# Kernel optimization log

Measured on AMD Instinct MI355X. Metric: run time of the kernel, lower is better.

The kernel has to match this reference:

```python
import jax, jax.numpy as jnp
import numpy as np

H, D = 12, 128          # heads, head_dim
DIM = 1536              # vid_dim == txt_dim == H*D
EPS = 1e-6


def _rmsnorm(x, w):
    # RMSNorm over last dim (head_dim) with learnable scale
    var = jnp.mean(jnp.square(x), axis=-1, keepdims=True)
    return x * jax.lax.rsqrt(var + EPS) * w


def setup_inputs() -> dict:
    key = jax.random.key(0)
    ks = jax.random.split(key, 16)
    B, Lv, Lt = 2, 2 * 24 * 40, 128
    inner = H * D
    s = 0.02
    inp = {
        "vid": jax.random.normal(ks[0], (B * Lv, DIM), jnp.float32),
        "txt": jax.random.normal(ks[1], (B * Lt, DIM), jnp.float32),
        "Wqkv_vid": jax.random.normal(ks[2], (DIM, 3 * inner), jnp.float32) * s,
        "bqkv_vid": jnp.zeros((3 * inner,), jnp.float32),
        "Wqkv_txt": jax.random.normal(ks[3], (DIM, 3 * inner), jnp.float32) * s,
        "bqkv_txt": jnp.zeros((3 * inner,), jnp.float32),
        "nq_vid": jnp.ones((D,), jnp.float32),
        "nk_vid": jnp.ones((D,), jnp.float32),
        "nq_txt": jnp.ones((D,), jnp.float32),
        "nk_txt": jnp.ones((D,), jnp.float32),
        "Wout_vid": jax.random.normal(ks[4], (inner, DIM), jnp.float32) * s,
        "bout_vid": jnp.zeros((DIM,), jnp.float32),
        "Wout_txt": jax.random.normal(ks[5], (inner, DIM), jnp.float32) * s,
        "bout_txt": jnp.zeros((DIM,), jnp.float32),
        # static per-sample shapes (numpy => usable as Python ints under jit)
        "vid_shape": np.array([[2, 24, 40], [2, 24, 40]], np.int64),
        "txt_shape": np.array([[128], [128]], np.int64),
    }
    return inp


def reference(vid, txt, Wqkv_vid, bqkv_vid, Wqkv_txt, bqkv_txt,
              nq_vid, nk_vid, nq_txt, nk_txt,
              Wout_vid, bout_vid, Wout_txt, bout_txt,
              vid_shape, txt_shape):
    B = vid_shape.shape[0]
    Lv = int(np.prod(vid_shape[0]))   # equal lengths across batch
    Lt = int(txt_shape[0, 0])

    # fused QKV projections (separate weights for vid/txt, shared_weights=False)
    vid_qkv = (vid @ Wqkv_vid + bqkv_vid).reshape(-1, 3, H, D)
    txt_qkv = (txt @ Wqkv_txt + bqkv_txt).reshape(-1, 3, H, D)
    vq, vk, vv = vid_qkv[:, 0], vid_qkv[:, 1], vid_qkv[:, 2]
    tq, tk, tv = txt_qkv[:, 0], txt_qkv[:, 1], txt_qkv[:, 2]

    # QK-norm (per-modality RMSNorm over head_dim)
    vq, tq = _rmsnorm(vq, nq_vid), _rmsnorm(tq, nq_txt)
    vk, tk = _rmsnorm(vk, nk_vid), _rmsnorm(tk, nk_txt)

    # multimodal packing: per sample, vid tokens then txt tokens (cu_seqlens over vid_len+txt_len)
    def pack(v, t):
        v = v.reshape(B, Lv, H, D)
        t = t.reshape(B, Lt, H, D)
        return jnp.concatenate([v, t], axis=1)  # [B, Lv+Lt, H, D]

    q = pack(vq, tq).astype(jnp.bfloat16)
    k = pack(vk, tk).astype(jnp.bfloat16)
    v = pack(vv, tv).astype(jnp.bfloat16)

    scale = 1.0 / np.sqrt(D)
    scores = jnp.einsum('blhd,bmhd->bhlm', q, k,
                        preferred_element_type=jnp.float32) * scale
    probs = jax.nn.softmax(scores, axis=-1)
    out = jnp.einsum('bhlm,bmhd->blhd', probs.astype(jnp.bfloat16), v,
                     preferred_element_type=jnp.float32).astype(vid.dtype)

    # unconcat + head merge
    out = out.reshape(B, Lv + Lt, H * D)
    vid_out = out[:, :Lv].reshape(B * Lv, H * D)
    txt_out = out[:, Lv:].reshape(B * Lt, H * D)

    vid_out = vid_out @ Wout_vid + bout_vid
    txt_out = txt_out @ Wout_txt + bout_txt
    return (vid_out, txt_out)
```

## Files before the change

### kernel.cpp

```cpp
#include <hip/hip_runtime.h>
#include <hip/hip_bf16.h>
#include <stdint.h>

typedef __attribute__((ext_vector_type(8))) short  short8;
typedef __attribute__((ext_vector_type(4))) float  f32x4;
typedef __attribute__((ext_vector_type(4))) unsigned int uint4v;
typedef __attribute__((ext_vector_type(4))) unsigned short ushort4v;

#define MFMA16(a,b,c) __builtin_amdgcn_mfma_f32_16x16x32_bf16((a),(b),(c),0,0,0)

#define AS1 __attribute__((address_space(1)))
#define AS3 __attribute__((address_space(3)))
static __device__ __forceinline__ void gload16(void* lds, const void* g) {
  __builtin_amdgcn_global_load_lds((AS1 const void*)g, (AS3 void*)lds, 16, 0, 0);
}

static __device__ __forceinline__ unsigned short f2bf(float x) {
  unsigned int u = __float_as_uint(x);
  u += 0x7fffu + ((u >> 16) & 1u);
  return (unsigned short)(u >> 16);
}
static __device__ __forceinline__ float bf2f(unsigned short h) {
  return __uint_as_float(((unsigned int)h) << 16);
}

#define HDS   12
#define DD    128
#define DIMK  1536
#define NIN   4608
#define LV    1920
#define LT    128
#define LL    2048
#define BB    2
#define MV    3840
#define MT    256
#define MTOT  4096

__global__ __launch_bounds__(256) void split_x(const float* __restrict__ vid,
                                               const float* __restrict__ txt,
                                               unsigned short* __restrict__ xhi) {
  size_t i = ((size_t)blockIdx.x * 256 + threadIdx.x) * 4;
  const size_t NV = (size_t)MV * DIMK;
  const float* src = (i < NV) ? (vid + i) : (txt + (i - NV));
  f32x4 v = *(const f32x4*)src;
  ushort4v hv;
#pragma unroll
  for (int j = 0; j < 4; ++j) hv[j] = f2bf(v[j]);
  *(ushort4v*)(xhi + i) = hv;
}

__global__ __launch_bounds__(256) void transpose_cast(const float* __restrict__ W,
                                                      unsigned short* __restrict__ Thi,
                                                      int K, int N) {
  __shared__ float tile[32][33];
  const int tx = threadIdx.x & 31, ty = threadIdx.x >> 5;
  const int k0 = blockIdx.y * 32, n0 = blockIdx.x * 32;
#pragma unroll
  for (int i = 0; i < 32; i += 8)
    tile[ty + i][tx] = W[(size_t)(k0 + ty + i) * N + n0 + tx];
  __syncthreads();
#pragma unroll
  for (int i = 0; i < 32; i += 8)
    Thi[(size_t)(n0 + ty + i) * K + k0 + tx] = f2bf(tile[tx][ty + i]);
}

__global__ __launch_bounds__(256) void vt_transpose(const unsigned short* __restrict__ v,
                                                    unsigned short* __restrict__ vtb) {
  __shared__ unsigned short tile[32][33];
  const int tx = threadIdx.x & 31, ty = threadIdx.x >> 5;
  const int bh = blockIdx.z;
  const int l0 = blockIdx.x * 32, d0 = blockIdx.y * 32;
  const size_t base = (size_t)bh * LL * DD;
#pragma unroll
  for (int i = 0; i < 32; i += 8)
    tile[ty + i][tx] = v[base + (size_t)(l0 + ty + i) * DD + d0 + tx];
  __syncthreads();
#pragma unroll
  for (int i = 0; i < 32; i += 8)
    vtb[base + (size_t)(d0 + ty + i) * LL + l0 + tx] = tile[tx][ty + i];
}

__device__ __forceinline__ void bf16_mainloop256(
    const unsigned short* __restrict__ Ahi, const unsigned short* __restrict__ Bhi,
    int m0, int n0,
    uint4v* __restrict__ sA, uint4v* __restrict__ sB,
    f32x4 (&acc)[4][4]) {
  const int t = threadIdx.x;
  const int lane = t & 63;
  const int w = t >> 6;
  const int wm = w >> 1, wn = w & 1;
  const int lr = lane & 15, lg = lane >> 4;
  const int ra = t >> 1, ca = (t & 1) * 2;
  const int rb = t >> 2, cb = t & 3;
  const size_t arow = (size_t)(m0 + ra) * DIMK + ca * 8;
  const size_t brow = (size_t)(n0 + rb) * DIMK + cb * 8;
  const int sa0 = ca * 256 + ra, sa1 = (ca + 1) * 256 + ra;
  const int sb0 = cb * 128 + rb;
  const int fA = lg * 256 + wm * 64 + lr;
  const int fB = lg * 128 + wn * 64 + lr;

  uint4v va0 = *(const uint4v*)(Ahi + arow);
  uint4v va1 = *(const uint4v*)(Ahi + arow + 8);
  uint4v vb0 = *(const uint4v*)(Bhi + brow);

  int cur = 0;
  for (int k0 = 0; k0 < DIMK; k0 += 32) {
    const int ha = cur * 1024, hb = cur * 512;
    sA[ha + sa0] = va0; sA[ha + sa1] = va1;
    sB[hb + sb0] = vb0;
    if (k0 + 32 < DIMK) {
      va0 = *(const uint4v*)(Ahi + arow + k0 + 32);
      va1 = *(const uint4v*)(Ahi + arow + k0 + 40);
      vb0 = *(const uint4v*)(Bhi + brow + k0 + 32);
    }
    __syncthreads();
    short8 ah[4], bh[4];
#pragma unroll
    for (int i = 0; i < 4; ++i) {
      ah[i] = *(const short8*)&sA[ha + fA + i * 16];
      bh[i] = *(const short8*)&sB[hb + fB + i * 16];
    }
#pragma unroll
    for (int mi = 0; mi < 4; ++mi)
#pragma unroll
      for (int ni = 0; ni < 4; ++ni)
        acc[mi][ni] = MFMA16(ah[mi], bh[ni], acc[mi][ni]);
    cur ^= 1;
  }
}

__global__ __launch_bounds__(512) void gemm_qkv(
    const unsigned short* __restrict__ Xhi,
    const unsigned short* __restrict__ WvH, const unsigned short* __restrict__ WtH,
    const float* __restrict__ bias_v, const float* __restrict__ bias_t,
    const float* __restrict__ nq_v, const float* __restrict__ nk_v,
    const float* __restrict__ nq_t, const float* __restrict__ nk_t,
    unsigned short* __restrict__ qb, unsigned short* __restrict__ kb,
    unsigned short* __restrict__ vb) {
  __shared__ uint4v sA[2048], sB[1024];
  __shared__ float rowsq[2][256];
  const int t = threadIdx.x;
  const int lane = t & 63;
  const int w = t >> 6;
  const int wm = w >> 1, wn = w & 1;
  const int lr = lane & 15, lg = lane >> 4;
  const int bid = blockIdx.x;
  const int xcd = bid & 7, ii = bid >> 3;
  const int mt = xcd * 2 + (ii & 1), nt = ii >> 1;
  const int m0 = mt * 256, n0 = nt * 128;
  const bool istxt = (m0 >= MV);
  const unsigned short* WThi = istxt ? WtH : WvH;
  const float* bias = istxt ? bias_t : bias_v;
  const int Lmod = istxt ? LT : LV;
  const int loff = istxt ? LV : 0;
  const int mbase = istxt ? MV : 0;

  f32x4 acc[4][4];
#pragma unroll
  for (int mi = 0; mi < 4; ++mi)
#pragma unroll
    for (int ni = 0; ni < 4; ++ni) acc[mi][ni] = (f32x4){0.f, 0.f, 0.f, 0.f};

  bf16_mainloop256(Xhi, WThi, m0, n0, sA, sB, acc);

  const int s  = n0 / DIMK;
  const int hh = (n0 % DIMK) / DD;
#pragma unroll
  for (int ni = 0; ni < 4; ++ni) {
    float bv = bias[n0 + wn * 64 + ni * 16 + lr];
#pragma unroll
    for (int mi = 0; mi < 4; ++mi)
#pragma unroll
      for (int r = 0; r < 4; ++r) acc[mi][ni][r] += bv;
  }
  if (s < 2) {
    __syncthreads();
#pragma unroll
    for (int mi = 0; mi < 4; ++mi)
#pragma unroll
      for (int r = 0; r < 4; ++r) {
        float p = 0.f;
#pragma unroll
        for (int ni = 0; ni < 4; ++ni) p += acc[mi][ni][r] * acc[mi][ni][r];
        p += __shfl_xor(p, 1); p += __shfl_xor(p, 2);
        p += __shfl_xor(p, 4); p += __shfl_xor(p, 8);
        if (lr == 0) rowsq[wn][wm * 64 + mi * 16 + lg * 4 + r] = p;
      }
    __syncthreads();
    const float* nw = (s == 0) ? (istxt ? nq_t : nq_v) : (istxt ? nk_t : nk_v);
    float nwv[4];
#pragma unroll
    for (int ni = 0; ni < 4; ++ni) nwv[ni] = nw[wn * 64 + ni * 16 + lr];
#pragma unroll
    for (int mi = 0; mi < 4; ++mi)
#pragma unroll
      for (int r = 0; r < 4; ++r) {
        int row = wm * 64 + mi * 16 + lg * 4 + r;
        float a = (rowsq[0][row] + rowsq[1][row]) * (1.f / 128.f) + 1e-6f;
        float x = rsqrtf(a);
        x = x * (1.5f - 0.5f * a * x * x);
#pragma unroll
        for (int ni = 0; ni < 4; ++ni) acc[mi][ni][r] *= x * nwv[ni];
      }
  }
  unsigned short* dst = (s == 0) ? qb : ((s == 1) ? kb : vb);
#pragma unroll
  for (int mi = 0; mi < 4; ++mi)
#pragma unroll
    for (int r = 0; r < 4; ++r) {
      int mrow = m0 + wm * 64 + mi * 16 + lg * 4 + r - mbase;
      int bidx = (mrow >= Lmod) ? 1 : 0;
      int l = loff + mrow - bidx * Lmod;
      size_t rb2 = ((size_t)(bidx * HDS + hh) * LL + l) * DD;
#pragma unroll
      for (int ni = 0; ni < 4; ++ni) {
        int d = wn * 64 + ni * 16 + lr;
        dst[rb2 + d] = f2bf(acc[mi][ni][r]);
      }
    }
}

__global__ __launch_bounds__(256) void attn_kernel(
    const unsigned short* __restrict__ qb, const unsigned short* __restrict__ kb,
    const unsigned short* __restrict__ vt,
    unsigned short* __restrict__ aohi) {
  const int t = threadIdx.x;
  const int lane = t & 63, w = t >> 6;
  const int lr = lane & 15, lg = lane >> 4;
  const int bid = blockIdx.x;
  const int xcd = bid & 7, ii = bid >> 3;
  const int bh = xcd * 3 + (ii >> 5);
  const int qt = ii & 31;
  const int q0 = (qt * 4 + w) * 16;
  const size_t base = (size_t)bh * LL * DD;
  const float scale = 0.08838834764831845f;

  __shared__ __align__(16) unsigned short Kbuf[2][32 * 128];
  __shared__ __align__(16) unsigned short Vbuf[2][128 * 32];
  __shared__ __align__(16) unsigned short P[4][16 * 40];

  const char* kglob = (const char*)(kb + base);
  const char* vglob = (const char*)(vt + base);
  auto stageK = [&](int kt, int buf) {
    const char* gk = kglob + (size_t)kt * 32 * DD * 2;
#pragma unroll
    for (int is = 0; is < 2; ++is) {
      int Bl = is * 4096 + t * 16;
      int Bu = is * 4096 + w * 1024;
      int src = Bl ^ (((Bl >> 8) & 7) << 4);
      gload16((char*)Kbuf[buf] + Bu, gk + src);
    }
  };
  auto stageV = [&](int kt, int buf) {
    const char* gv = vglob + kt * 64;
#pragma unroll
    for (int is = 0; is < 2; ++is) {
      int Bl = is * 4096 + t * 16;
      int Bu = is * 4096 + w * 1024;
      int row = Bl >> 6;
      int ch  = ((Bl >> 4) & 3) ^ (row & 3);
      gload16((char*)Vbuf[buf] + Bu, gv + (size_t)row * (LL * 2) + ch * 16);
    }
  };
  auto readK = [&](int buf, int rr, int ks) -> short8 {
    int byte = rr * 256 + ((ks * 64 + lg * 16) ^ ((rr & 7) << 4));
    return *(const short8*)((const char*)Kbuf[buf] + byte);
  };
  auto readV = [&](int buf, int df) -> short8 {
    int row = df * 16 + lr;
    int byte = row * 64 + ((lg ^ (row & 3)) << 4);
    return *(const short8*)((const char*)Vbuf[buf] + byte);
  };

  short8 qf[4];
#pragma unroll
  for (int ks = 0; ks < 4; ++ks)
    qf[ks] = *(const short8*)(qb + base + (size_t)(q0 + lr) * DD + ks * 32 + lg * 8);

  f32x4 o[8];
#pragma unroll
  for (int i = 0; i < 8; ++i) o[i] = (f32x4){0.f, 0.f, 0.f, 0.f};
  float Z[4] = {0.f, 0.f, 0.f, 0.f};

  stageK(0, 0); stageV(0, 0);
  __syncthreads();
  for (int kt = 0; kt < LL / 32; ++kt) {
    const int cur = kt & 1;
    if (kt + 1 < LL / 32) { stageK(kt + 1, cur ^ 1); stageV(kt + 1, cur ^ 1); }
    f32x4 s0a = (f32x4){0.f, 0.f, 0.f, 0.f}, s0b = (f32x4){0.f, 0.f, 0.f, 0.f};
    f32x4 s1a = (f32x4){0.f, 0.f, 0.f, 0.f}, s1b = (f32x4){0.f, 0.f, 0.f, 0.f};
#pragma unroll
    for (int ks = 0; ks < 4; ++ks) {
      short8 k0f = readK(cur, lr, ks);
      short8 k1f = readK(cur, 16 + lr, ks);
      if (ks < 2) { s0a = MFMA16(qf[ks], k0f, s0a); s1a = MFMA16(qf[ks], k1f, s1a); }
      else        { s0b = MFMA16(qf[ks], k0f, s0b); s1b = MFMA16(qf[ks], k1f, s1b); }
    }
#pragma unroll
    for (int r = 0; r < 4; ++r) {
      float p0 = __expf((s0a[r] + s0b[r]) * scale);
      float p1 = __expf((s1a[r] + s1b[r]) * scale);
      Z[r] += p0 + p1;
      P[w][(lg * 4 + r) * 40 + lr]      = f2bf(p0);
      P[w][(lg * 4 + r) * 40 + 16 + lr] = f2bf(p1);
    }
    short8 pa = *(const short8*)&P[w][lr * 40 + lg * 8];
#pragma unroll
    for (int df = 0; df < 8; ++df) {
      short8 vf = readV(cur, df);
      o[df] = MFMA16(pa, vf, o[df]);
    }
    __syncthreads();
  }

  float invZ[4];
#pragma unroll
  for (int r = 0; r < 4; ++r) {
    Z[r] += __shfl_xor(Z[r], 1); Z[r] += __shfl_xor(Z[r], 2);
    Z[r] += __shfl_xor(Z[r], 4); Z[r] += __shfl_xor(Z[r], 8);
    invZ[r] = 1.0f / Z[r];
  }

  const int b = bh / HDS, h = bh % HDS;
#pragma unroll
  for (int df = 0; df < 8; ++df)
#pragma unroll
    for (int r = 0; r < 4; ++r) {
      int l = q0 + lg * 4 + r;
      size_t row = (l < LV) ? ((size_t)b * LV + l) : ((size_t)MV + b * LT + (l - LV));
      int col = h * DD + df * 16 + lr;
      aohi[row * DIMK + col] = f2bf(o[df][r] * invZ[r]);
    }
}

__device__ __forceinline__ void bf16_mainloop128(
    const unsigned short* __restrict__ Ahi, const unsigned short* __restrict__ Bhi,
    int m0, int n0,
    uint4v* __restrict__ sA, uint4v* __restrict__ sB,
    f32x4 (&acc)[4][4]) {
  const int t = threadIdx.x;
  const int lane = t & 63;
  const int w = t >> 6;
  const int wm = w >> 1, wn = w & 1;
  const int lr = lane & 15, lg = lane >> 4;
  const int sr = t >> 1;
  const int sc = (t & 1) * 2;
  const size_t arow = (size_t)(m0 + sr) * DIMK + sc * 8;
  const size_t brow = (size_t)(n0 + sr) * DIMK + sc * 8;
  const int slot0 = sc * 128 + sr, slot1 = (sc + 1) * 128 + sr;
  const int fA = lg * 128 + wm * 64 + lr;
  const int fB = lg * 128 + wn * 64 + lr;

  uint4v va0 = *(const uint4v*)(Ahi + arow);
  uint4v va1 = *(const uint4v*)(Ahi + arow + 8);
  uint4v vb0 = *(const uint4v*)(Bhi + brow);
  uint4v vb1 = *(const uint4v*)(Bhi + brow + 8);

  int cur = 0;
  for (int k0 = 0; k0 < DIMK; k0 += 32) {
    const int hs = cur * 512;
    sA[hs + slot0] = va0; sA[hs + slot1] = va1;
    sB[hs + slot0] = vb0; sB[hs + slot1] = vb1;
    if (k0 + 32 < DIMK) {
      va0 = *(const uint4v*)(Ahi + arow + k0 + 32);
      va1 = *(const uint4v*)(Ahi + arow + k0 + 40);
      vb0 = *(const uint4v*)(Bhi + brow + k0 + 32);
      vb1 = *(const uint4v*)(Bhi + brow + k0 + 40);
    }
    __syncthreads();
    short8 ah[4], bh[4];
#pragma unroll
    for (int i = 0; i < 4; ++i) {
      ah[i] = *(const short8*)&sA[hs + fA + i * 16];
      bh[i] = *(const short8*)&sB[hs + fB + i * 16];
    }
#pragma unroll
    for (int mi = 0; mi < 4; ++mi)
#pragma unroll
      for (int ni = 0; ni < 4; ++ni)
        acc[mi][ni] = MFMA16(ah[mi], bh[ni], acc[mi][ni]);
    cur ^= 1;
  }
}

__global__ __launch_bounds__(256) void gemm_out(
    const unsigned short* __restrict__ Ahi,
    const unsigned short* __restrict__ WvH, const unsigned short* __restrict__ WtH,
    const float* __restrict__ bias_v, const float* __restrict__ bias_t,
    float* __restrict__ out) {
  __shared__ uint4v sA[1024], sB[1024];
  const int t = threadIdx.x;
  const int lane = t & 63;
  const int w = t >> 6;
  const int wm = w >> 1, wn = w & 1;
  const int lr = lane & 15, lg = lane >> 4;
  const int bid = blockIdx.x;
  const int xcd = bid & 7, ii = bid >> 3;
  const int mt = xcd * 4 + (ii & 3), nt = ii >> 2;
  const int m0 = mt * 128, n0 = nt * 128;
  const bool istxt = (m0 >= MV);
  const unsigned short* WThi = istxt ? WtH : WvH;
  const float* bias = istxt ? bias_t : bias_v;

  f32x4 acc[4][4];
#pragma unroll
  for (int mi = 0; mi < 4; ++mi)
#pragma unroll
    for (int ni = 0; ni < 4; ++ni) acc[mi][ni] = (f32x4){0.f, 0.f, 0.f, 0.f};

  bf16_mainloop128(Ahi, WThi, m0, n0, sA, sB, acc);

#pragma unroll
  for (int ni = 0; ni < 4; ++ni) {
    float bv = bias[n0 + wn * 64 + ni * 16 + lr];
#pragma unroll
    for (int mi = 0; mi < 4; ++mi)
#pragma unroll
      for (int r = 0; r < 4; ++r) {
        size_t row = (size_t)(m0 + wm * 64 + mi * 16 + lg * 4 + r);
        out[row * DIMK + n0 + wn * 64 + ni * 16 + lr] = acc[mi][ni][r] + bv;
      }
  }
}

extern "C" void kernel_launch(void* const* d_in, const int* in_sizes, int n_in,
                              void* d_out, int out_size, void* d_ws, size_t ws_size,
                              hipStream_t stream) {
  (void)in_sizes; (void)n_in; (void)out_size; (void)ws_size;
  const float* vid      = (const float*)d_in[0];
  const float* txt      = (const float*)d_in[1];
  const float* Wqkv_vid = (const float*)d_in[2];
  const float* bqkv_vid = (const float*)d_in[3];
  const float* Wqkv_txt = (const float*)d_in[4];
  const float* bqkv_txt = (const float*)d_in[5];
  const float* nq_vid   = (const float*)d_in[6];
  const float* nk_vid   = (const float*)d_in[7];
  const float* nq_txt   = (const float*)d_in[8];
  const float* nk_txt   = (const float*)d_in[9];
  const float* Wout_vid = (const float*)d_in[10];
  const float* bout_vid = (const float*)d_in[11];
  const float* Wout_txt = (const float*)d_in[12];
  const float* bout_txt = (const float*)d_in[13];
  float* out = (float*)d_out;

  char* ws = (char*)d_ws;
  size_t off = 0;
  auto alloc = [&](size_t bytes) { char* p = ws + off; off += (bytes + 255) & ~(size_t)255; return p; };

  const size_t SZ_X    = (size_t)MTOT * DIMK * 2;
  const size_t SZ_WQKV = (size_t)NIN * DIMK * 2;
  const size_t SZ_WOUT = (size_t)DIMK * DIMK * 2;
  const size_t SZ_QKVB = (size_t)BB * HDS * LL * DD * 2;

  unsigned short* Xhi   = (unsigned short*)alloc(SZ_X);
  unsigned short* WTqvH = (unsigned short*)alloc(SZ_WQKV);
  unsigned short* WTqtH = (unsigned short*)alloc(SZ_WQKV);
  unsigned short* WTovH = (unsigned short*)alloc(SZ_WOUT);
  unsigned short* WTotH = (unsigned short*)alloc(SZ_WOUT);
  unsigned short* QB    = (unsigned short*)alloc(SZ_QKVB);
  unsigned short* KB    = (unsigned short*)alloc(SZ_QKVB);
  unsigned short* VB    = (unsigned short*)alloc(SZ_QKVB);
  unsigned short* VT    = WTqvH;
  unsigned short* AOhi  = Xhi;

  split_x<<<dim3((MTOT * DIMK) / (256 * 4)), dim3(256), 0, stream>>>(vid, txt, Xhi);
  transpose_cast<<<dim3(NIN / 32, DIMK / 32), dim3(256), 0, stream>>>(Wqkv_vid, WTqvH, DIMK, NIN);
  transpose_cast<<<dim3(NIN / 32, DIMK / 32), dim3(256), 0, stream>>>(Wqkv_txt, WTqtH, DIMK, NIN);
  transpose_cast<<<dim3(DIMK / 32, DIMK / 32), dim3(256), 0, stream>>>(Wout_vid, WTovH, DIMK, DIMK);
  transpose_cast<<<dim3(DIMK / 32, DIMK / 32), dim3(256), 0, stream>>>(Wout_txt, WTotH, DIMK, DIMK);
  gemm_qkv<<<dim3(576), dim3(512), 0, stream>>>(
      Xhi, WTqvH, WTqtH, bqkv_vid, bqkv_txt,
      nq_vid, nk_vid, nq_txt, nk_txt, QB, KB, VB);
  vt_transpose<<<dim3(LL / 32, DD / 32, BB * HDS), dim3(256), 0, stream>>>(VB, VT);
  attn_kernel<<<dim3(768), dim3(256), 0, stream>>>(QB, KB, VT, AOhi);
  gemm_out<<<dim3(384), dim3(256), 0, stream>>>(
      AOhi, WTovH, WTotH, bout_vid, bout_txt, out);
}
```

Measured before the change: 243.6 us.

## Fold softmax scale and log2e into Q norm; use raw exp2 and packed bf16 conversion

The attention scale and the log2(e) factor are folded into the Q RMSNorm weights in the QKV kernel. The attention loop can then call the hardware v_exp_f32 (exp2) directly, with no per-element multiply. Probabilities are packed two at a time with v_cvt_pk_bf16_f32 into an interleaved P layout, which halves the LDS stores. K rows are reordered so each lane's pair of keys sits next to each other. LDS and global staging addresses are precomputed outside the loop and the loop is unrolled by two, which cuts integer address arithmetic in the hot loop. The cost is that Q is stored in bf16 already scaled, which shifts rounding slightly.

```diff
diff --git a/kernel.cpp b/kernel.cpp
--- a/kernel.cpp
+++ b/kernel.cpp
@@ -35,6 +35,7 @@
 #define MV    3840
 #define MT    256
 #define MTOT  4096
+#define QSC   (0.08838834764831845f * 1.4426950408889634f)
 
 __global__ __launch_bounds__(256) void split_x(const float* __restrict__ vid,
                                                const float* __restrict__ txt,
@@ -188,9 +189,10 @@
       }
     __syncthreads();
     const float* nw = (s == 0) ? (istxt ? nq_t : nq_v) : (istxt ? nk_t : nk_v);
+    const float post = (s == 0) ? QSC : 1.0f;
     float nwv[4];
 #pragma unroll
-    for (int ni = 0; ni < 4; ++ni) nwv[ni] = nw[wn * 64 + ni * 16 + lr];
+    for (int ni = 0; ni < 4; ++ni) nwv[ni] = nw[wn * 64 + ni * 16 + lr] * post;
 #pragma unroll
     for (int mi = 0; mi < 4; ++mi)
 #pragma unroll
@@ -233,7 +235,6 @@
   const int qt = ii & 31;
   const int q0 = (qt * 4 + w) * 16;
   const size_t base = (size_t)bh * LL * DD;
-  const float scale = 0.08838834764831845f;
 
   __shared__ __align__(16) unsigned short Kbuf[2][32 * 128];
   __shared__ __align__(16) unsigned short Vbuf[2][128 * 32];
@@ -241,36 +242,29 @@
 
   const char* kglob = (const char*)(kb + base);
   const char* vglob = (const char*)(vt + base);
-  auto stageK = [&](int kt, int buf) {
-    const char* gk = kglob + (size_t)kt * 32 * DD * 2;
-#pragma unroll
-    for (int is = 0; is < 2; ++is) {
-      int Bl = is * 4096 + t * 16;
-      int Bu = is * 4096 + w * 1024;
-      int src = Bl ^ (((Bl >> 8) & 7) << 4);
-      gload16((char*)Kbuf[buf] + Bu, gk + src);
-    }
-  };
-  auto stageV = [&](int kt, int buf) {
-    const char* gv = vglob + kt * 64;
-#pragma unroll
-    for (int is = 0; is < 2; ++is) {
-      int Bl = is * 4096 + t * 16;
-      int Bu = is * 4096 + w * 1024;
-      int row = Bl >> 6;
-      int ch  = ((Bl >> 4) & 3) ^ (row & 3);
-      gload16((char*)Vbuf[buf] + Bu, gv + (size_t)row * (LL * 2) + ch * 16);
-    }
-  };
-  auto readK = [&](int buf, int rr, int ks) -> short8 {
-    int byte = rr * 256 + ((ks * 64 + lg * 16) ^ ((rr & 7) << 4));
-    return *(const short8*)((const char*)Kbuf[buf] + byte);
-  };
-  auto readV = [&](int buf, int df) -> short8 {
-    int row = df * 16 + lr;
-    int byte = row * 64 + ((lg ^ (row & 3)) << 4);
-    return *(const short8*)((const char*)Vbuf[buf] + byte);
-  };
+
+  const int  srcK  = (t * 16) ^ (((t >> 4) & 7) << 4);
+  const size_t vs0 = (size_t)(t >> 2) * (LL * 2) +
+                     (((t & 3) ^ ((t >> 2) & 3)) << 4);
+  const size_t vs1 = vs0 + (size_t)64 * (LL * 2);
+  char* kd0 = (char*)Kbuf + w * 1024;
+  char* kd1 = kd0 + 4096;
+  char* vd0 = (char*)Vbuf + w * 1024;
+  char* vd1 = vd0 + 4096;
+
+  int akr[2][4];
+#pragma unroll
+  for (int h = 0; h < 2; ++h) {
+    const int rr = 2 * lr + h;
+#pragma unroll
+    for (int ks = 0; ks < 4; ++ks)
+      akr[h][ks] = rr * 256 + ((ks * 64 + lg * 16) ^ ((rr & 7) << 4));
+  }
+  const int av0 = lr * 64 + ((lg ^ (lr & 3)) << 4);
+  char* pwr = (char*)P + w * 1280 + lg * 320 + lr * 4;
+  const char* prd = (const char*)P + w * 1280 + lr * 80 + lg * 16;
+  const char* KB = (const char*)Kbuf;
+  const char* VB = (const char*)Vbuf;
 
   short8 qf[4];
 #pragma unroll
@@ -282,35 +276,53 @@
   for (int i = 0; i < 8; ++i) o[i] = (f32x4){0.f, 0.f, 0.f, 0.f};
   float Z[4] = {0.f, 0.f, 0.f, 0.f};
 
-  stageK(0, 0); stageV(0, 0);
+  const char* gkp = kglob;
+  const char* gvp = vglob;
+  gload16(kd0, gkp + srcK);
+  gload16(kd1, gkp + 4096 + srcK);
+  gload16(vd0, gvp + vs0);
+  gload16(vd1, gvp + vs1);
   __syncthreads();
+
+#pragma unroll 2
   for (int kt = 0; kt < LL / 32; ++kt) {
     const int cur = kt & 1;
-    if (kt + 1 < LL / 32) { stageK(kt + 1, cur ^ 1); stageV(kt + 1, cur ^ 1); }
+    const int cb = cur * 8192, nb = (cur ^ 1) * 8192;
+    if (kt + 1 < LL / 32) {
+      gload16(kd0 + nb, gkp + 8192 + srcK);
+      gload16(kd1 + nb, gkp + 8192 + 4096 + srcK);
+      gload16(vd0 + nb, gvp + 64 + vs0);
+      gload16(vd1 + nb, gvp + 64 + vs1);
+    }
     f32x4 s0a = (f32x4){0.f, 0.f, 0.f, 0.f}, s0b = (f32x4){0.f, 0.f, 0.f, 0.f};
     f32x4 s1a = (f32x4){0.f, 0.f, 0.f, 0.f}, s1b = (f32x4){0.f, 0.f, 0.f, 0.f};
 #pragma unroll
     for (int ks = 0; ks < 4; ++ks) {
-      short8 k0f = readK(cur, lr, ks);
-      short8 k1f = readK(cur, 16 + lr, ks);
+      short8 k0f = *(const short8*)(KB + cb + akr[0][ks]);
+      short8 k1f = *(const short8*)(KB + cb + akr[1][ks]);
       if (ks < 2) { s0a = MFMA16(qf[ks], k0f, s0a); s1a = MFMA16(qf[ks], k1f, s1a); }
       else        { s0b = MFMA16(qf[ks], k0f, s0b); s1b = MFMA16(qf[ks], k1f, s1b); }
     }
 #pragma unroll
     for (int r = 0; r < 4; ++r) {
-      float p0 = __expf((s0a[r] + s0b[r]) * scale);
-      float p1 = __expf((s1a[r] + s1b[r]) * scale);
+      float p0, p1;
+      float sa = s0a[r] + s0b[r];
+      float sb = s1a[r] + s1b[r];
+      asm("v_exp_f32 %0, %1" : "=v"(p0) : "v"(sa));
+      asm("v_exp_f32 %0, %1" : "=v"(p1) : "v"(sb));
       Z[r] += p0 + p1;
-      P[w][(lg * 4 + r) * 40 + lr]      = f2bf(p0);
-      P[w][(lg * 4 + r) * 40 + 16 + lr] = f2bf(p1);
-    }
-    short8 pa = *(const short8*)&P[w][lr * 40 + lg * 8];
+      unsigned int u;
+      asm("v_cvt_pk_bf16_f32 %0, %1, %2" : "=v"(u) : "v"(p0), "v"(p1));
+      *(unsigned int*)(pwr + r * 80) = u;
+    }
+    short8 pa = *(const short8*)prd;
 #pragma unroll
     for (int df = 0; df < 8; ++df) {
-      short8 vf = readV(cur, df);
+      short8 vf = *(const short8*)(VB + cb + df * 1024 + av0);
       o[df] = MFMA16(pa, vf, o[df]);
     }
     __syncthreads();
+    gkp += 8192; gvp += 64;
   }
 
   float invZ[4];
```

Result: faster. 230.3 us (-5.5%).
